# Kernel tuning notes

Measured on AMD Instinct MI355X. Metric: run time of the kernel, lower is better.

Reference implementation:

```python
import jax, jax.numpy as jnp
import numpy as np

# Static architecture of the decoded CNN (matches init_kwargs index_dict)
KERNEL_NO = [64, 128, 256]
KERNEL_SIZE = [9, 9, 9]
CH_IN = [3, 64, 128]
IDX_START = [0, 1792, 75648]
I_DIM = 370816  # last slice's last index + 1
D_MODEL = 512
BATCH = 128
N_LAYERS = len(KERNEL_NO)


def _build_slices():
    """Replicates DebedderNeuron.get_kernel_slices(); per-layer int32 index matrix [K_l, L_l]."""
    sl = []
    for idx in range(N_LAYERS):
        rows = []
        for kd in range(KERNEL_NO[idx]):
            s = IDX_START[idx] + kd * KERNEL_SIZE[idx] * CH_IN[idx]
            e = s + KERNEL_SIZE[idx] * CH_IN[idx]
            bias = IDX_START[idx] + KERNEL_NO[idx] * KERNEL_SIZE[idx] * CH_IN[idx] + kd
            ik = list(range(s, e)) + [bias]
            if idx < N_LAYERS - 1:
                for kn in range(KERNEL_NO[idx + 1]):
                    ns = (IDX_START[idx + 1] + kd * KERNEL_SIZE[idx + 1]
                          + kn * CH_IN[idx + 1] * KERNEL_SIZE[idx + 1])
                    ik.extend(range(ns, ns + KERNEL_SIZE[idx + 1]))
            rows.append(ik)
        sl.append(jnp.asarray(np.array(rows, dtype=np.int32)))
    return sl

IDX = _build_slices()  # lengths per row: [1180, 2881, 1153]


def setup_inputs() -> dict:
    key = jax.random.key(0)
    ks = jax.random.split(key, 7)
    dims = [int(IDX[l].shape[1]) for l in range(N_LAYERS)]
    inp = {"x": jax.random.normal(ks[0], (BATCH, sum(KERNEL_NO), D_MODEL), jnp.float32)}
    for l in range(N_LAYERS):
        inp[f"W{l}"] = jax.random.normal(ks[1 + 2 * l], (D_MODEL, dims[l]), jnp.float32) * 0.02
        inp[f"b{l}"] = jax.random.normal(ks[2 + 2 * l], (dims[l],), jnp.float32) * 0.02
    return inp


def reference(x, W0, b0, W1, b1, W2, b2):
    # One shared Linear per CNN layer (as in the torch module); batch all kernels of a
    # layer into a single GEMM, then scatter-add into the flat weight vector y.
    Ws = [W0, W1, W2]
    bs = [b0, b1, b2]
    y = jnp.zeros((x.shape[0], I_DIM), x.dtype)
    off = 0
    for l in range(N_LAYERS):
        K = KERNEL_NO[l]
        yt = jnp.einsum('bkd,di->bki', x[:, off:off + K], Ws[l]) + bs[l]  # [B, K_l, L_l]
        y = y.at[:, IDX[l]].add(yt)  # overlapping scatter-add, matches sequential += in torch
        off += K
    # middle layers are written twice (own slice + previous layer's extension) -> halve
    y = y.at[:, IDX_START[1]:IDX_START[-1]].multiply(0.5)
    return y
```

## Files before the change

kernel.cpp:

```cpp
#include <hip/hip_runtime.h>
#include <cstdint>

typedef short short8 __attribute__((ext_vector_type(8)));
typedef float f32x4 __attribute__((ext_vector_type(4)));

#define LDS_AS3(p) ((__attribute__((address_space(3))) unsigned*)(p))
#define GLB_AS1(p) ((const __attribute__((address_space(1))) unsigned*)(p))

__device__ inline unsigned bfpack(float a, float b) {
    union { float f; unsigned u; } ua, ub;
    ua.f = a; ub.f = b;
    unsigned lo = (ua.u + 0x7FFFu + ((ua.u >> 16) & 1u)) >> 16;
    unsigned hi = (ub.u + 0x7FFFu + ((ub.u >> 16) & 1u)) & 0xFFFF0000u;
    return lo | hi;
}
__device__ inline unsigned short bf16of(float a) { return (unsigned short)bfpack(a, 0.0f); }
__device__ inline float bf2f(unsigned short s) {
    union { unsigned u; float f; } x; x.u = (unsigned)s << 16; return x.f;
}

__global__ __launch_bounds__(256)
void cvt_x(const float* __restrict__ X, unsigned short* __restrict__ XB)
{
    const int g = blockIdx.x * 256 + threadIdx.x;
    const float4 v0 = *(const float4*)(X + (size_t)g * 8);
    const float4 v1 = *(const float4*)(X + (size_t)g * 8 + 4);
    uint4 u;
    u.x = bfpack(v0.x, v0.y); u.y = bfpack(v0.z, v0.w);
    u.z = bfpack(v1.x, v1.y); u.w = bfpack(v1.z, v1.w);
    *(uint4*)(XB + (size_t)g * 8) = u;
}

template <int N>
__global__ __launch_bounds__(256)
void cvt_w(const float* __restrict__ W, unsigned short* __restrict__ WT)
{
    const int g = blockIdx.x * 256 + threadIdx.x;
    if (g >= N * 64) return;
    const int n = g % N, d8 = g / N;
    const float* p = W + (size_t)d8 * 8 * N + n;
    uint4 u;
    u.x = bfpack(p[0],             p[(size_t)N]);
    u.y = bfpack(p[2 * (size_t)N], p[3 * (size_t)N]);
    u.z = bfpack(p[4 * (size_t)N], p[5 * (size_t)N]);
    u.w = bfpack(p[6 * (size_t)N], p[7 * (size_t)N]);
    *(uint4*)(WT + (size_t)n * 512 + d8 * 8) = u;
}

template <int MODE, bool FUSED>
__global__ __launch_bounds__(256)
void gemm_scatter(const unsigned short* __restrict__ XB,
                  const unsigned short* __restrict__ WT,
                  const float* __restrict__ BIAS, float* __restrict__ Y,
                  const unsigned short* __restrict__ EXTI,
                  unsigned short* __restrict__ EXTO)
{
    constexpr int K_L  = (MODE == 0) ? 64 : (MODE == 1) ? 128 : 256;
    constexpr int LOGK = (MODE == 0) ? 6  : (MODE == 1) ? 7   : 8;
    constexpr int N    = (MODE == 0) ? 1180 : (MODE == 1) ? 2881 : 1153;
    constexpr int XOFF = (MODE == 0) ? 0 : (MODE == 1) ? 64 : 192;
    constexpr int NT   = (N + 127) / 128;

    __shared__ __align__(16) unsigned short lA[3][128 * 32];
    __shared__ __align__(16) unsigned short lB[3][128 * 32];

    const int t    = threadIdx.x;
    const int lane = t & 63;
    const int wave = t >> 6;
    const int wr   = wave >> 1, wc = wave & 1;

    const int cpx = (int)gridDim.x >> 3;
    const int wg  = (blockIdx.x & 7) * cpx + (blockIdx.x >> 3);
    const int nt  = wg % NT;
    const int mt  = wg / NT;
    const int m0  = mt * 128;
    const int n0  = nt * 128;

    f32x4 acc[4][4] = {};

    auto stage = [&](int buf, int kk) {
        #pragma unroll
        for (int i = 0; i < 2; ++i) {
            const int cidx = i * 256 + t;
            const int row  = cidx >> 2;
            const int kgl  = (cidx & 3) ^ ((row >> 1) & 3);
            const int m    = m0 + row;
            const int b    = m >> LOGK;
            const int kd   = m & (K_L - 1);
            const unsigned short* gp =
                XB + ((size_t)(b * 448 + XOFF + kd) << 9) + kk + kgl * 8;
            __builtin_amdgcn_global_load_lds(GLB_AS1(gp), LDS_AS3(&lA[buf][cidx * 8]), 16, 0, 0);
        }
        #pragma unroll
        for (int i = 0; i < 2; ++i) {
            const int cidx = i * 256 + t;
            const int row  = cidx >> 2;
            const int kgl  = (cidx & 3) ^ ((row >> 1) & 3);
            int gc = n0 + row; if (gc > N - 1) gc = N - 1;
            const unsigned short* gp = WT + (size_t)gc * 512 + kk + kgl * 8;
            __builtin_amdgcn_global_load_lds(GLB_AS1(gp), LDS_AS3(&lB[buf][cidx * 8]), 16, 0, 0);
        }
    };

    stage(0, 0);
    stage(1, 32);

    int cur = 0;
    #pragma unroll 1
    for (int ks = 0; ks < 16; ++ks) {
        if (ks == 15) asm volatile("s_waitcnt vmcnt(0)" ::: "memory");
        else          asm volatile("s_waitcnt vmcnt(4)" ::: "memory");
        __builtin_amdgcn_s_barrier();

        const int kgl  = lane >> 4;
        const int lr16 = lane & 15;
        short8 af[4], bfr[4];
        #pragma unroll
        for (int mi = 0; mi < 4; ++mi) {
            const int row = wr * 64 + mi * 16 + lr16;
            af[mi] = *(const short8*)(&lA[cur][(row * 4 + (kgl ^ ((row >> 1) & 3))) * 8]);
        }
        #pragma unroll
        for (int ni = 0; ni < 4; ++ni) {
            const int row = wc * 64 + ni * 16 + lr16;
            bfr[ni] = *(const short8*)(&lB[cur][(row * 4 + (kgl ^ ((row >> 1) & 3))) * 8]);
        }

        if (ks < 14) {
            int b2 = cur + 2; if (b2 >= 3) b2 -= 3;
            stage(b2, (ks + 2) * 32);
        }

        #pragma unroll
        for (int mi = 0; mi < 4; ++mi)
            #pragma unroll
            for (int ni = 0; ni < 4; ++ni)
                acc[mi][ni] = __builtin_amdgcn_mfma_f32_16x16x32_bf16(
                    af[mi], bfr[ni], acc[mi][ni], 0, 0, 0);

        cur = (cur + 1 == 3) ? 0 : cur + 1;
    }

    const int lr = lane & 15;
    const int lq = lane >> 4;
    #pragma unroll
    for (int ni = 0; ni < 4; ++ni) {
        const int n = n0 + wc * 64 + ni * 16 + lr;
        if (n >= N) continue;
        const float bias = BIAS[n];
        #pragma unroll
        for (int mi = 0; mi < 4; ++mi) {
            #pragma unroll
            for (int r = 0; r < 4; ++r) {
                const int m  = m0 + wr * 64 + mi * 16 + lq * 4 + r;
                const int b  = m >> LOGK;
                const int kd = m & (K_L - 1);
                const float v = acc[mi][ni][r] + bias;
                float* yb = Y + (size_t)b * 370816;
                if constexpr (FUSED) {
                    if constexpr (MODE == 0) {
                        if (n < 27)       yb[kd * 27 + n] = v;
                        else if (n == 27) yb[1728 + kd]   = v;
                        else EXTO[((size_t)(b * 64 + kd)) * 1152 + (n - 28)] = bf16of(v);
                    } else if constexpr (MODE == 1) {
                        if (n < 576) {
                            const float e = bf2f(EXTI[((size_t)(b * 64 + n / 9)) * 1152 + kd * 9 + n % 9]);
                            yb[1792 + kd * 576 + n] = 0.5f * (v + e);
                        } else if (n == 576) yb[75520 + kd] = 0.5f * v;
                        else EXTO[((size_t)(b * 128 + kd)) * 2304 + (n - 577)] = bf16of(v);
                    } else {
                        if (n < 1152) {
                            const float e = bf2f(EXTI[((size_t)(b * 128 + n / 9)) * 2304 + kd * 9 + n % 9]);
                            yb[75648 + kd * 1152 + n] = v + e;
                        } else yb[370560 + kd] = v;
                    }
                } else {
                    if constexpr (MODE == 0) {
                        if (n < 27)       yb[kd * 27 + n] = v;
                        else if (n == 27) yb[1728 + kd]   = v;
                        else {
                            int tt = n - 28, kn = tt / 9, j = tt - kn * 9;
                            yb[1792 + kn * 576 + kd * 9 + j] = 0.5f * v;
                        }
                    } else if constexpr (MODE == 1) {
                        if (n < 576)       yb[1792 + kd * 576 + n] += 0.5f * v;
                        else if (n == 576) yb[75520 + kd] = 0.5f * v;
                        else {
                            int tt = n - 577, kn = tt / 9, j = tt - kn * 9;
                            yb[75648 + kn * 1152 + kd * 9 + j] = v;
                        }
                    } else {
                        if (n < 1152) yb[75648 + kd * 1152 + n] += v;
                        else          yb[370560 + kd] = v;
                    }
                }
            }
        }
    }
}

extern "C" void kernel_launch(void* const* d_in, const int* in_sizes, int n_in,
                              void* d_out, int out_size, void* d_ws, size_t ws_size,
                              hipStream_t stream)
{
    const float* x  = (const float*)d_in[0];
    const float* W0 = (const float*)d_in[1];
    const float* b0 = (const float*)d_in[2];
    const float* W1 = (const float*)d_in[3];
    const float* b1 = (const float*)d_in[4];
    const float* W2 = (const float*)d_in[5];
    const float* b2 = (const float*)d_in[6];
    float* y = (float*)d_out;

    unsigned short* XB   = (unsigned short*)d_ws;
    unsigned short* WT0  = XB   + (size_t)128 * 448 * 512;
    unsigned short* WT1  = WT0  + (size_t)1180 * 512;
    unsigned short* WT2  = WT1  + (size_t)2881 * 512;
    unsigned short* EXT0 = WT2  + (size_t)1153 * 512;
    unsigned short* EXT1 = EXT0 + (size_t)128 * 64 * 1152;
    const size_t NEED_FUSED =
        ((size_t)128 * 448 * 512 + (size_t)5214 * 512 +
         (size_t)128 * 64 * 1152 + (size_t)128 * 128 * 2304) * 2;

    cvt_x<<<dim3(14336), 256, 0, stream>>>(x, XB);
    cvt_w<1180><<<dim3((1180 * 64 + 255) / 256), 256, 0, stream>>>(W0, WT0);
    cvt_w<2881><<<dim3((2881 * 64 + 255) / 256), 256, 0, stream>>>(W1, WT1);
    cvt_w<1153><<<dim3((1153 * 64 + 255) / 256), 256, 0, stream>>>(W2, WT2);

    if (ws_size >= NEED_FUSED) {
        gemm_scatter<0, true><<<dim3(64 * 10),  256, 0, stream>>>(XB, WT0, b0, y, nullptr, EXT0);
        gemm_scatter<1, true><<<dim3(128 * 23), 256, 0, stream>>>(XB, WT1, b1, y, EXT0, EXT1);
        gemm_scatter<2, true><<<dim3(256 * 10), 256, 0, stream>>>(XB, WT2, b2, y, EXT1, nullptr);
    } else {
        gemm_scatter<0, false><<<dim3(64 * 10),  256, 0, stream>>>(XB, WT0, b0, y, nullptr, nullptr);
        gemm_scatter<1, false><<<dim3(128 * 23), 256, 0, stream>>>(XB, WT1, b1, y, nullptr, nullptr);
        gemm_scatter<2, false><<<dim3(256 * 10), 256, 0, stream>>>(XB, WT2, b2, y, nullptr, nullptr);
    }
}
```

Measured before the change: 302.2 us.

## Enlarge GEMM tiles to 256x256 with 8 waves and phased double buffering

Switches the GEMM-scatter kernels from 128x128 tiles with 4 waves and a triple-buffered 32-wide k pipeline to 256x256 tiles with 8 waves, 64-wide k steps, double buffering split into half-tile loads interleaved across four compute phases, and s_setprio around MFMA bursts. It aims to raise operand reuse and MFMA density per load. It also removes the non-fused fallback path, always using the bf16 extension buffers. Trade-offs: far fewer blocks (160 for layer 0), large LDS footprint limiting occupancy, and extra barriers per k step.

```diff
diff --git a/kernel.cpp b/kernel.cpp
--- a/kernel.cpp
+++ b/kernel.cpp
@@ -47,8 +47,8 @@
     *(uint4*)(WT + (size_t)n * 512 + d8 * 8) = u;
 }
 
-template <int MODE, bool FUSED>
-__global__ __launch_bounds__(256)
+template <int MODE>
+__global__ __launch_bounds__(512, 2)
 void gemm_scatter(const unsigned short* __restrict__ XB,
                   const unsigned short* __restrict__ WT,
                   const float* __restrict__ BIAS, float* __restrict__ Y,
@@ -59,140 +59,131 @@
     constexpr int LOGK = (MODE == 0) ? 6  : (MODE == 1) ? 7   : 8;
     constexpr int N    = (MODE == 0) ? 1180 : (MODE == 1) ? 2881 : 1153;
     constexpr int XOFF = (MODE == 0) ? 0 : (MODE == 1) ? 64 : 192;
-    constexpr int NT   = (N + 127) / 128;
-
-    __shared__ __align__(16) unsigned short lA[3][128 * 32];
-    __shared__ __align__(16) unsigned short lB[3][128 * 32];
+    constexpr int NT   = (N + 255) / 256;
+
+    __shared__ __align__(16) unsigned short lA[2 * 2 * 128 * 64];
+    __shared__ __align__(16) unsigned short lB[2 * 2 * 128 * 64];
 
     const int t    = threadIdx.x;
     const int lane = t & 63;
-    const int wave = t >> 6;
-    const int wr   = wave >> 1, wc = wave & 1;
+    const int wv   = t >> 6;
+    const int wr   = wv >> 2;
+    const int wc   = wv & 3;
+    const int kq   = lane >> 4;
+    const int lr16 = lane & 15;
 
     const int cpx = (int)gridDim.x >> 3;
     const int wg  = (blockIdx.x & 7) * cpx + (blockIdx.x >> 3);
     const int nt  = wg % NT;
     const int mt  = wg / NT;
-    const int m0  = mt * 128;
-    const int n0  = nt * 128;
-
-    f32x4 acc[4][4] = {};
-
-    auto stage = [&](int buf, int kk) {
+    const int m0  = mt * 256;
+    const int n0  = nt * 256;
+
+    f32x4 acc[8][4] = {};
+
+    auto stageHalf = [&](int buf, int op , int half, int kt) {
         #pragma unroll
-        for (int i = 0; i < 2; ++i) {
-            const int cidx = i * 256 + t;
-            const int row  = cidx >> 2;
-            const int kgl  = (cidx & 3) ^ ((row >> 1) & 3);
-            const int m    = m0 + row;
-            const int b    = m >> LOGK;
-            const int kd   = m & (K_L - 1);
-            const unsigned short* gp =
-                XB + ((size_t)(b * 448 + XOFF + kd) << 9) + kk + kgl * 8;
-            __builtin_amdgcn_global_load_lds(GLB_AS1(gp), LDS_AS3(&lA[buf][cidx * 8]), 16, 0, 0);
-        }
-        #pragma unroll
-        for (int i = 0; i < 2; ++i) {
-            const int cidx = i * 256 + t;
-            const int row  = cidx >> 2;
-            const int kgl  = (cidx & 3) ^ ((row >> 1) & 3);
-            int gc = n0 + row; if (gc > N - 1) gc = N - 1;
-            const unsigned short* gp = WT + (size_t)gc * 512 + kk + kgl * 8;
-            __builtin_amdgcn_global_load_lds(GLB_AS1(gp), LDS_AS3(&lB[buf][cidx * 8]), 16, 0, 0);
+        for (int rnd = 0; rnd < 2; ++rnd) {
+            const int c   = rnd * 512 + t;
+            const int row = c >> 3;
+            const int l   = (c & 7) ^ (row & 7);
+            const unsigned short* gp;
+            if (op == 0) {
+                const int m = m0 + half * 128 + row;
+                const int b = m >> LOGK, kd = m & (K_L - 1);
+                gp = XB + ((size_t)(b * 448 + XOFF + kd) << 9) + kt * 64 + l * 8;
+            } else {
+                int gc = n0 + half * 128 + row; if (gc > N - 1) gc = N - 1;
+                gp = WT + (size_t)gc * 512 + kt * 64 + l * 8;
+            }
+            unsigned short* dst = (op ? lB : lA) + (size_t)(buf * 2 + half) * (128 * 64) + c * 8;
+            __builtin_amdgcn_global_load_lds(GLB_AS1(gp), LDS_AS3(dst), 16, 0, 0);
         }
     };
 
-    stage(0, 0);
-    stage(1, 32);
-
-    int cur = 0;
+    stageHalf(0, 0, 0, 0);
+    stageHalf(0, 1, 0, 0);
+    stageHalf(0, 0, 1, 0);
+    stageHalf(0, 1, 1, 0);
+    asm volatile("s_waitcnt vmcnt(0)" ::: "memory");
+    __builtin_amdgcn_s_barrier();
+
     #pragma unroll 1
-    for (int ks = 0; ks < 16; ++ks) {
-        if (ks == 15) asm volatile("s_waitcnt vmcnt(0)" ::: "memory");
-        else          asm volatile("s_waitcnt vmcnt(4)" ::: "memory");
-        __builtin_amdgcn_s_barrier();
-
-        const int kgl  = lane >> 4;
-        const int lr16 = lane & 15;
-        short8 af[4], bfr[4];
+    for (int kt = 0; kt < 8; ++kt) {
+        const int buf = kt & 1;
+        const char* Abase = (const char*)lA + (size_t)(buf * 2 + wr) * (128 * 128);
+        const char* Bbase = (const char*)lB + (size_t)(buf * 2 + (wc >> 1)) * (128 * 128);
+
         #pragma unroll
-        for (int mi = 0; mi < 4; ++mi) {
-            const int row = wr * 64 + mi * 16 + lr16;
-            af[mi] = *(const short8*)(&lA[cur][(row * 4 + (kgl ^ ((row >> 1) & 3))) * 8]);
+        for (int ph = 0; ph < 4; ++ph) {
+            const int mq = ph >> 1, ks = ph & 1;
+
+            short8 af[4], bf[4];
+            #pragma unroll
+            for (int mi = 0; mi < 4; ++mi) {
+                const int row  = mq * 64 + mi * 16 + lr16;
+                const int slot = (ks * 4 + kq) ^ (row & 7);
+                af[mi] = *(const short8*)(Abase + row * 128 + slot * 16);
+            }
+            #pragma unroll
+            for (int ni = 0; ni < 4; ++ni) {
+                const int row  = (wc & 1) * 64 + ni * 16 + lr16;
+                const int slot = (ks * 4 + kq) ^ (row & 7);
+                bf[ni] = *(const short8*)(Bbase + row * 128 + slot * 16);
+            }
+
+            if (ph == 0) {
+                if (kt + 1 < 8) { stageHalf(buf ^ 1, 0, 0, kt + 1);
+                                  stageHalf(buf ^ 1, 1, 0, kt + 1); }
+            } else if (ph == 1) {
+                if (kt + 1 < 8) { stageHalf(buf ^ 1, 0, 1, kt + 1);
+                                  stageHalf(buf ^ 1, 1, 1, kt + 1); }
+            } else if (ph == 3) {
+                asm volatile("s_waitcnt vmcnt(0)" ::: "memory");
+            }
+
+            __builtin_amdgcn_s_barrier();
+            __builtin_amdgcn_s_setprio(1);
+            #pragma unroll
+            for (int mi = 0; mi < 4; ++mi)
+                #pragma unroll
+                for (int ni = 0; ni < 4; ++ni)
+                    acc[mq * 4 + mi][ni] = __builtin_amdgcn_mfma_f32_16x16x32_bf16(
+                        af[mi], bf[ni], acc[mq * 4 + mi][ni], 0, 0, 0);
+            __builtin_amdgcn_s_setprio(0);
+            __builtin_amdgcn_s_barrier();
         }
-        #pragma unroll
-        for (int ni = 0; ni < 4; ++ni) {
-            const int row = wc * 64 + ni * 16 + lr16;
-            bfr[ni] = *(const short8*)(&lB[cur][(row * 4 + (kgl ^ ((row >> 1) & 3))) * 8]);
-        }
-
-        if (ks < 14) {
-            int b2 = cur + 2; if (b2 >= 3) b2 -= 3;
-            stage(b2, (ks + 2) * 32);
-        }
-
-        #pragma unroll
-        for (int mi = 0; mi < 4; ++mi)
-            #pragma unroll
-            for (int ni = 0; ni < 4; ++ni)
-                acc[mi][ni] = __builtin_amdgcn_mfma_f32_16x16x32_bf16(
-                    af[mi], bfr[ni], acc[mi][ni], 0, 0, 0);
-
-        cur = (cur + 1 == 3) ? 0 : cur + 1;
     }
 
-    const int lr = lane & 15;
-    const int lq = lane >> 4;
     #pragma unroll
     for (int ni = 0; ni < 4; ++ni) {
-        const int n = n0 + wc * 64 + ni * 16 + lr;
+        const int n = n0 + wc * 64 + ni * 16 + lr16;
         if (n >= N) continue;
         const float bias = BIAS[n];
         #pragma unroll
-        for (int mi = 0; mi < 4; ++mi) {
+        for (int mi = 0; mi < 8; ++mi) {
             #pragma unroll
             for (int r = 0; r < 4; ++r) {
-                const int m  = m0 + wr * 64 + mi * 16 + lq * 4 + r;
+                const int m  = m0 + wr * 128 + mi * 16 + kq * 4 + r;
                 const int b  = m >> LOGK;
                 const int kd = m & (K_L - 1);
                 const float v = acc[mi][ni][r] + bias;
                 float* yb = Y + (size_t)b * 370816;
-                if constexpr (FUSED) {
-                    if constexpr (MODE == 0) {
-                        if (n < 27)       yb[kd * 27 + n] = v;
-                        else if (n == 27) yb[1728 + kd]   = v;
-                        else EXTO[((size_t)(b * 64 + kd)) * 1152 + (n - 28)] = bf16of(v);
-                    } else if constexpr (MODE == 1) {
-                        if (n < 576) {
-                            const float e = bf2f(EXTI[((size_t)(b * 64 + n / 9)) * 1152 + kd * 9 + n % 9]);
-                            yb[1792 + kd * 576 + n] = 0.5f * (v + e);
-                        } else if (n == 576) yb[75520 + kd] = 0.5f * v;
-                        else EXTO[((size_t)(b * 128 + kd)) * 2304 + (n - 577)] = bf16of(v);
-                    } else {
-                        if (n < 1152) {
-                            const float e = bf2f(EXTI[((size_t)(b * 128 + n / 9)) * 2304 + kd * 9 + n % 9]);
-                            yb[75648 + kd * 1152 + n] = v + e;
-                        } else yb[370560 + kd] = v;
-                    }
+                if constexpr (MODE == 0) {
+                    if (n < 27)       yb[kd * 27 + n] = v;
+                    else if (n == 27) yb[1728 + kd]   = v;
+                    else EXTO[((size_t)(b * 64 + kd)) * 1152 + (n - 28)] = bf16of(v);
+                } else if constexpr (MODE == 1) {
+                    if (n < 576) {
+                        const float e = bf2f(EXTI[((size_t)(b * 64 + n / 9)) * 1152 + kd * 9 + n % 9]);
+                        yb[1792 + kd * 576 + n] = 0.5f * (v + e);
+                    } else if (n == 576) yb[75520 + kd] = 0.5f * v;
+                    else EXTO[((size_t)(b * 128 + kd)) * 2304 + (n - 577)] = bf16of(v);
                 } else {
-                    if constexpr (MODE == 0) {
-                        if (n < 27)       yb[kd * 27 + n] = v;
-                        else if (n == 27) yb[1728 + kd]   = v;
-                        else {
-                            int tt = n - 28, kn = tt / 9, j = tt - kn * 9;
-                            yb[1792 + kn * 576 + kd * 9 + j] = 0.5f * v;
-                        }
-                    } else if constexpr (MODE == 1) {
-                        if (n < 576)       yb[1792 + kd * 576 + n] += 0.5f * v;
-                        else if (n == 576) yb[75520 + kd] = 0.5f * v;
-                        else {
-                            int tt = n - 577, kn = tt / 9, j = tt - kn * 9;
-                            yb[75648 + kn * 1152 + kd * 9 + j] = v;
-                        }
-                    } else {
-                        if (n < 1152) yb[75648 + kd * 1152 + n] += v;
-                        else          yb[370560 + kd] = v;
-                    }
+                    if (n < 1152) {
+                        const float e = bf2f(EXTI[((size_t)(b * 128 + n / 9)) * 2304 + kd * 9 + n % 9]);
+                        yb[75648 + kd * 1152 + n] = v + e;
+                    } else yb[370560 + kd] = v;
                 }
             }
         }
@@ -218,22 +209,13 @@
     unsigned short* WT2  = WT1  + (size_t)2881 * 512;
     unsigned short* EXT0 = WT2  + (size_t)1153 * 512;
     unsigned short* EXT1 = EXT0 + (size_t)128 * 64 * 1152;
-    const size_t NEED_FUSED =
-        ((size_t)128 * 448 * 512 + (size_t)5214 * 512 +
-         (size_t)128 * 64 * 1152 + (size_t)128 * 128 * 2304) * 2;
 
     cvt_x<<<dim3(14336), 256, 0, stream>>>(x, XB);
     cvt_w<1180><<<dim3((1180 * 64 + 255) / 256), 256, 0, stream>>>(W0, WT0);
     cvt_w<2881><<<dim3((2881 * 64 + 255) / 256), 256, 0, stream>>>(W1, WT1);
     cvt_w<1153><<<dim3((1153 * 64 + 255) / 256), 256, 0, stream>>>(W2, WT2);
 
-    if (ws_size >= NEED_FUSED) {
-        gemm_scatter<0, true><<<dim3(64 * 10),  256, 0, stream>>>(XB, WT0, b0, y, nullptr, EXT0);
-        gemm_scatter<1, true><<<dim3(128 * 23), 256, 0, stream>>>(XB, WT1, b1, y, EXT0, EXT1);
-        gemm_scatter<2, true><<<dim3(256 * 10), 256, 0, stream>>>(XB, WT2, b2, y, EXT1, nullptr);
-    } else {
-        gemm_scatter<0, false><<<dim3(64 * 10),  256, 0, stream>>>(XB, WT0, b0, y, nullptr, nullptr);
-        gemm_scatter<1, false><<<dim3(128 * 23), 256, 0, stream>>>(XB, WT1, b1, y, nullptr, nullptr);
-        gemm_scatter<2, false><<<dim3(256 * 10), 256, 0, stream>>>(XB, WT2, b2, y, nullptr, nullptr);
-    }
-}
+    gemm_scatter<0><<<dim3(32 * 5),   512, 0, stream>>>(XB, WT0, b0, y, nullptr, EXT0);
+    gemm_scatter<1><<<dim3(64 * 12),  512, 0, stream>>>(XB, WT1, b1, y, EXT0, EXT1);
+    gemm_scatter<2><<<dim3(128 * 5),  512, 0, stream>>>(XB, WT2, b2, y, EXT1, nullptr);
+}
```

Result: slower. 366.4 us (+21.2%).
